# Optimization experiments

Hardware: AMD Instinct MI355X
Metric: run time of the kernel (lower is better)

Reference implementation:

```python
import jax, jax.numpy as jnp
import numpy as np

N_NODES = 50000
N_EDGES = 50000  # per-node attention scores are used as per-hyperedge weights => M == N
IN_CH = 128
OUT_CH = 128
NNZ = 800000


def setup_inputs() -> dict:
    key = jax.random.key(0)
    k = jax.random.split(key, 7)
    x = jax.random.normal(k[0], (N_NODES, IN_CH), dtype=jnp.float32)
    node_idx = jax.random.randint(k[1], (NNZ,), 0, N_NODES)
    edge_idx = jax.random.randint(k[2], (NNZ,), 0, N_EDGES)
    hyperedge_index = jnp.stack([node_idx, edge_idx]).astype(jnp.int64)
    s_in = 1.0 / np.sqrt(IN_CH)
    attn_w = jax.random.uniform(k[3], (1, IN_CH), minval=-s_in, maxval=s_in, dtype=jnp.float32)
    attn_b = jax.random.uniform(k[4], (1,), minval=-s_in, maxval=s_in, dtype=jnp.float32)
    lin_w = jax.random.uniform(k[5], (OUT_CH, IN_CH), minval=-s_in, maxval=s_in, dtype=jnp.float32)
    bias = jax.random.uniform(k[6], (OUT_CH,), minval=-s_in, maxval=s_in, dtype=jnp.float32)
    return {"x": x, "hyperedge_index": hyperedge_index,
            "attn_w": attn_w, "attn_b": attn_b, "lin_w": lin_w, "bias": bias}


def reference(x, hyperedge_index, attn_w, attn_b, lin_w, bias):
    # x: [N, C_in]; hyperedge_index: [2, nnz] (row 0: node ids, row 1: hyperedge ids)
    node_idx = hyperedge_index[0]
    edge_idx = hyperedge_index[1]
    N = x.shape[0]
    M = N_EDGES

    # edge_weight = sigmoid(attn(x)) -> used as hyperedge_weight (per-edge, M == N)
    w = jax.nn.sigmoid(x @ attn_w.T + attn_b)[:, 0]            # [M]

    xl = x @ lin_w.T                                           # [N, C_out]

    # D_v = sum of incident hyperedge weights per node; D^{-1} with inf -> 0
    D = jax.ops.segment_sum(w[edge_idx], node_idx, num_segments=N)
    Dinv = jnp.where(D > 0, 1.0 / D, 0.0)                      # [N]

    # B_e = hyperedge degree; B^{-1} with inf -> 0
    ones = jnp.ones(edge_idx.shape, dtype=x.dtype)
    Bdeg = jax.ops.segment_sum(ones, edge_idx, num_segments=M)
    Binv = jnp.where(Bdeg > 0, 1.0 / Bdeg, 0.0)                # [M]

    # node -> hyperedge: message = B_e^{-1} * x_j, aggregated at edge e
    msg = Binv[edge_idx][:, None] * xl[node_idx]               # [nnz, C_out]
    e_feat = jax.ops.segment_sum(msg, edge_idx, num_segments=M)

    # hyperedge -> node: message = D_v^{-1} * e_feat, aggregated at node v
    out = jax.ops.segment_sum(e_feat[edge_idx], node_idx, num_segments=N)
    out = Dinv[:, None] * out

    return out + bias
```

## Files before the change

### kernel.cpp

```cpp
#include <hip/hip_runtime.h>
#include <math.h>

#define CH 128
#define CAP 64
#define RSB 9
#define RS  (1 << RSB)
#define CAPB 10240
#define PB 2048
#define SUB 8
#define IDS 64

typedef __attribute__((ext_vector_type(8))) short bf16x8;
typedef __attribute__((ext_vector_type(4))) float f32x4;

__device__ __forceinline__ unsigned short f2bf(float f) {
    union { float f; unsigned u; } v; v.f = f;
    unsigned r = v.u + 0x7FFF + ((v.u >> 16) & 1);
    return (unsigned short)(r >> 16);
}
__device__ __forceinline__ float bflo(unsigned u) {
    union { unsigned u; float f; } v; v.u = u << 16; return v.f;
}
__device__ __forceinline__ float bfhi(unsigned u) {
    union { unsigned u; float f; } v; v.u = u & 0xFFFF0000u; return v.f;
}
__device__ __forceinline__ unsigned pack2bf(float a, float b) {
    return (unsigned)f2bf(a) | ((unsigned)f2bf(b) << 16);
}

__global__ __launch_bounds__(256) void fused_main(const float* __restrict__ x,
                                                  const float* __restrict__ attn_w,
                                                  const float* __restrict__ attn_b,
                                                  const float* __restrict__ lw,
                                                  unsigned short* __restrict__ xl,
                                                  float* __restrict__ w,
                                                  int nStrips,
                                                  const int* __restrict__ nidx,
                                                  const int* __restrict__ eidx,
                                                  int* __restrict__ binCnt,
                                                  unsigned int* __restrict__ binData,
                                                  int nnz, int nbd, int SB) {
    __shared__ unsigned short wl[128 * 136];
    __shared__ float awl[128];
    if ((int)blockIdx.x < SB) {
        int* hist = (int*)wl;
        int* base = ((int*)wl) + 256;
        int nbt = 2 * nbd;
        for (int i = threadIdx.x; i < nbt; i += 256) hist[i] = 0;
        __syncthreads();
        int k0 = blockIdx.x * PB + threadIdx.x;
        int vv[8], ee[8], sE[8], sN[8];
#pragma unroll
        for (int u = 0; u < 8; ++u) {
            int k = k0 + u * 256;
            if (k < nnz) {
                int v = nidx[k], e = eidx[k];
                vv[u] = v; ee[u] = e;
                sE[u] = atomicAdd(&hist[e >> RSB], 1);
                sN[u] = atomicAdd(&hist[nbd + (v >> RSB)], 1);
            } else vv[u] = -1;
        }
        __syncthreads();
        for (int i = threadIdx.x; i < nbt; i += 256)
            if (hist[i]) base[i] = atomicAdd(&binCnt[i], hist[i]);
        __syncthreads();
#pragma unroll
        for (int u = 0; u < 8; ++u) {
            if (vv[u] < 0) continue;
            int bE = ee[u] >> RSB;
            int bN = nbd + (vv[u] >> RSB);
            int iE = min(base[bE] + sE[u], CAPB - 1);
            int iN = min(base[bN] + sN[u], CAPB - 1);
            binData[(size_t)bE * CAPB + iE] = ((unsigned)ee[u] << 16) | (unsigned)vv[u];
            binData[(size_t)bN * CAPB + iN] = ((unsigned)vv[u] << 16) | (unsigned)ee[u];
        }
        return;
    }
    int tid = threadIdx.x;
    for (int i = tid; i < 2048; i += 256) {
        float4 vlo = ((const float4*)lw)[2 * i];
        float4 vhi = ((const float4*)lw)[2 * i + 1];
        int4 dst;
        dst.x = (int)pack2bf(vlo.x, vlo.y);
        dst.y = (int)pack2bf(vlo.z, vlo.w);
        dst.z = (int)pack2bf(vhi.x, vhi.y);
        dst.w = (int)pack2bf(vhi.z, vhi.w);
        *(int4*)(wl + (i >> 4) * 136 + (i & 15) * 8) = dst;
    }
    if (tid < 128) awl[tid] = attn_w[tid];
    float ab = attn_b[0];
    __syncthreads();
    int gb = blockIdx.x - SB;
    int wid = (gb << 2) | (tid >> 6);
    int lane = tid & 63;
    int m = lane & 15, quad = lane >> 4;
    int nWaves = ((int)gridDim.x - SB) << 2;
    for (int s = wid; s < nStrips; s += nWaves) {
        int r0 = s << 4;
        const float* xr = x + (size_t)(r0 + m) * CH + quad * 8;
        float att = 0.f;
        bf16x8 a0, a1, a2, a3;
#define LOAD_FRAG(AFRAG, F)                                                   \
        {                                                                     \
            float4 lo = *(const float4*)(xr + (F) * 32);                      \
            float4 hi = *(const float4*)(xr + (F) * 32 + 4);                  \
            const float* ap = &awl[(F) * 32 + quad * 8];                      \
            att += lo.x * ap[0] + lo.y * ap[1] + lo.z * ap[2] + lo.w * ap[3]  \
                 + hi.x * ap[4] + hi.y * ap[5] + hi.z * ap[6] + hi.w * ap[7]; \
            union { int4 i; bf16x8 v; } pk;                                   \
            pk.i.x = (int)pack2bf(lo.x, lo.y);                                \
            pk.i.y = (int)pack2bf(lo.z, lo.w);                                \
            pk.i.z = (int)pack2bf(hi.x, hi.y);                                \
            pk.i.w = (int)pack2bf(hi.z, hi.w);                                \
            AFRAG = pk.v;                                                     \
        }
        LOAD_FRAG(a0, 0)
        LOAD_FRAG(a1, 1)
        LOAD_FRAG(a2, 2)
        LOAD_FRAG(a3, 3)
#undef LOAD_FRAG
        att += __shfl_xor(att, 16, 64);
        att += __shfl_xor(att, 32, 64);
        if (quad == 0) w[r0 + m] = 1.0f / (1.0f + expf(-(att + ab)));
        unsigned short* orow = xl + (size_t)(r0 + quad * 4) * CH + m;
#pragma unroll
        for (int c0 = 0; c0 < 128; c0 += 16) {
            const unsigned short* wr = wl + (c0 + m) * 136 + quad * 8;
            f32x4 acc = {0.f, 0.f, 0.f, 0.f};
            acc = __builtin_amdgcn_mfma_f32_16x16x32_bf16(a0, *(const bf16x8*)(wr), acc, 0, 0, 0);
            acc = __builtin_amdgcn_mfma_f32_16x16x32_bf16(a1, *(const bf16x8*)(wr + 32), acc, 0, 0, 0);
            acc = __builtin_amdgcn_mfma_f32_16x16x32_bf16(a2, *(const bf16x8*)(wr + 64), acc, 0, 0, 0);
            acc = __builtin_amdgcn_mfma_f32_16x16x32_bf16(a3, *(const bf16x8*)(wr + 96), acc, 0, 0, 0);
            orow[c0]            = f2bf(acc[0]);
            orow[c0 + CH]       = f2bf(acc[1]);
            orow[c0 + 2 * CH]   = f2bf(acc[2]);
            orow[c0 + 3 * CH]   = f2bf(acc[3]);
        }
    }
}

__global__ __launch_bounds__(512) void edge_agg(const int* __restrict__ binCnt,
                                                const unsigned int* __restrict__ binData,
                                                const unsigned short* __restrict__ xl,
                                                unsigned short* __restrict__ ef, int M) {
    __shared__ unsigned short bucket[IDS * CAP];
    __shared__ int cl[IDS];
    int cb = blockIdx.x >> 3;
    int sr = blockIdx.x & (SUB - 1);
    int idBase = (cb << RSB) + (sr << 6);
    for (int i = threadIdx.x; i < IDS; i += 512) cl[i] = 0;
    __syncthreads();
    int n = min(binCnt[cb], CAPB);
    const unsigned int* src = binData + (size_t)cb * CAPB;
    for (int i = threadIdx.x; i < n; i += 512) {
        unsigned int entry = src[i];
        int lid = (int)(entry >> 16) - idBase;
        if ((unsigned)lid < IDS) {
            int r = atomicAdd(&cl[lid], 1);
            bucket[(lid << 6) + min(r, CAP - 1)] = (unsigned short)(entry & 0xFFFFu);
        }
    }
    __syncthreads();
    int wid = threadIdx.x >> 6, lane = threadIdx.x & 63;
    for (int li = wid; li < IDS; li += 8) {
        int gid = idBase + li;
        if (gid >= M) break;
        int deg = cl[li];
        int dl = min(deg, CAP);
        const unsigned short* col = bucket + (li << 6);
        float2 a0 = {0.f, 0.f}, a1 = {0.f, 0.f}, a2 = {0.f, 0.f}, a3 = {0.f, 0.f};
        int j = 0;
        for (; j + 3 < dl; j += 4) {
            int v0 = col[j], v1 = col[j + 1], v2 = col[j + 2], v3 = col[j + 3];
            unsigned u0 = *(const unsigned*)(xl + (size_t)v0 * CH + 2 * lane);
            unsigned u1 = *(const unsigned*)(xl + (size_t)v1 * CH + 2 * lane);
            unsigned u2 = *(const unsigned*)(xl + (size_t)v2 * CH + 2 * lane);
            unsigned u3 = *(const unsigned*)(xl + (size_t)v3 * CH + 2 * lane);
            a0.x += bflo(u0); a0.y += bfhi(u0);
            a1.x += bflo(u1); a1.y += bfhi(u1);
            a2.x += bflo(u2); a2.y += bfhi(u2);
            a3.x += bflo(u3); a3.y += bfhi(u3);
        }
        for (; j < dl; ++j) {
            unsigned u0 = *(const unsigned*)(xl + (size_t)col[j] * CH + 2 * lane);
            a0.x += bflo(u0); a0.y += bfhi(u0);
        }
        a0.x += a1.x + a2.x + a3.x;
        a0.y += a1.y + a2.y + a3.y;
        float binv = deg > 0 ? 1.0f / (float)deg : 0.0f;
        *(unsigned*)(ef + (size_t)gid * CH + 2 * lane) = pack2bf(a0.x * binv, a0.y * binv);
    }
}

__global__ __launch_bounds__(512) void node_agg(const int* __restrict__ binCnt,
                                                const unsigned int* __restrict__ binData,
                                                const unsigned short* __restrict__ ef,
                                                const float* __restrict__ w,
                                                const float* __restrict__ bias,
                                                float* __restrict__ out, int N) {
    __shared__ unsigned short bucket[IDS * CAP];
    __shared__ int cl[IDS];
    int cb = blockIdx.x >> 3;
    int sr = blockIdx.x & (SUB - 1);
    int idBase = (cb << RSB) + (sr << 6);
    for (int i = threadIdx.x; i < IDS; i += 512) cl[i] = 0;
    __syncthreads();
    int n = min(binCnt[cb], CAPB);
    const unsigned int* src = binData + (size_t)cb * CAPB;
    for (int i = threadIdx.x; i < n; i += 512) {
        unsigned int entry = src[i];
        int lid = (int)(entry >> 16) - idBase;
        if ((unsigned)lid < IDS) {
            int r = atomicAdd(&cl[lid], 1);
            bucket[(lid << 6) + min(r, CAP - 1)] = (unsigned short)(entry & 0xFFFFu);
        }
    }
    __syncthreads();
    int wid = threadIdx.x >> 6, lane = threadIdx.x & 63;
    for (int li = wid; li < IDS; li += 8) {
        int gid = idBase + li;
        if (gid >= N) break;
        int deg = cl[li];
        int dl = min(deg, CAP);
        const unsigned short* col = bucket + (li << 6);
        float2 a0 = {0.f, 0.f}, a1 = {0.f, 0.f}, a2 = {0.f, 0.f}, a3 = {0.f, 0.f};
        float ds = 0.f;
        int j = 0;
        for (; j + 3 < dl; j += 4) {
            int e0 = col[j], e1 = col[j + 1], e2 = col[j + 2], e3 = col[j + 3];
            unsigned u0 = *(const unsigned*)(ef + (size_t)e0 * CH + 2 * lane);
            unsigned u1 = *(const unsigned*)(ef + (size_t)e1 * CH + 2 * lane);
            unsigned u2 = *(const unsigned*)(ef + (size_t)e2 * CH + 2 * lane);
            unsigned u3 = *(const unsigned*)(ef + (size_t)e3 * CH + 2 * lane);
            ds += w[e0] + w[e1] + w[e2] + w[e3];
            a0.x += bflo(u0); a0.y += bfhi(u0);
            a1.x += bflo(u1); a1.y += bfhi(u1);
            a2.x += bflo(u2); a2.y += bfhi(u2);
            a3.x += bflo(u3); a3.y += bfhi(u3);
        }
        for (; j < dl; ++j) {
            int e0 = col[j];
            unsigned u0 = *(const unsigned*)(ef + (size_t)e0 * CH + 2 * lane);
            ds += w[e0];
            a0.x += bflo(u0); a0.y += bfhi(u0);
        }
        a0.x += a1.x + a2.x + a3.x;
        a0.y += a1.y + a2.y + a3.y;
        float dinv = ds > 0.f ? 1.0f / ds : 0.0f;
        float2 bi = *(const float2*)(bias + 2 * lane);
        float2 o = {a0.x * dinv + bi.x, a0.y * dinv + bi.y};
        *(float2*)(out + (size_t)gid * CH + 2 * lane) = o;
    }
}

extern "C" void kernel_launch(void* const* d_in, const int* in_sizes, int n_in,
                              void* d_out, int out_size, void* d_ws, size_t ws_size,
                              hipStream_t stream) {
    const float* x      = (const float*)d_in[0];
    const int*   hei    = (const int*)d_in[1];
    const float* attn_w = (const float*)d_in[2];
    const float* attn_b = (const float*)d_in[3];
    const float* lin_w  = (const float*)d_in[4];
    const float* bias   = (const float*)d_in[5];
    float* out = (float*)d_out;

    const int N   = in_sizes[0] / CH;
    const int nnz = in_sizes[1] / 2;
    const int* nidx = hei;
    const int* eidx = hei + nnz;

    unsigned short* efbf = (unsigned short*)d_ws;
    float*          w    = (float*)(efbf + (size_t)N * CH);
    unsigned int*   binData = (unsigned int*)(w + N);
    int nbd = (N + RS - 1) >> RSB;
    int*            binCnt  = (int*)(binData + (size_t)2 * nbd * CAPB);

    unsigned short* xlbf = (unsigned short*)out;

    hipMemsetAsync(binCnt, 0, (size_t)2 * nbd * sizeof(int), stream);

    int SB = (nnz + PB - 1) / PB;
    int nStrips = N / 16;
    int GB = (nStrips + 3) / 4;
    fused_main<<<SB + GB, 256, 0, stream>>>(x, attn_w, attn_b, lin_w, xlbf, w,
                                            nStrips, nidx, eidx, binCnt, binData,
                                            nnz, nbd, SB);

    edge_agg<<<nbd * SUB, 512, 0, stream>>>(binCnt, binData, xlbf, efbf, N);
    node_agg<<<nbd * SUB, 512, 0, stream>>>(binCnt + nbd,
                                            binData + (size_t)nbd * CAPB,
                                            efbf, w, bias, out, N);
}
```

Measured before the change: 180.3 us.

## Split wavefronts into half-waves gathering two rows each, double sub-bins per bin

Each wavefront now splits into two 32-lane halves that gather alternate neighbor rows with 8-byte loads, then combines them with a cross-half shuffle. The bin is split into 16 sub-ranges of 32 ids instead of 8 of 64, which doubles the block count, and the bin-scan loop reads entries as uint4. The goal is to raise memory-level parallelism and occupancy in the gather-bound aggregation kernels. In exchange, every block rescans the whole bin, so bin scanning is duplicated twice as often, and half the lanes sit idle during the final store.

```diff
diff --git a/kernel.cpp b/kernel.cpp
--- a/kernel.cpp
+++ b/kernel.cpp
@@ -7,8 +7,8 @@
 #define RS  (1 << RSB)
 #define CAPB 10240
 #define PB 2048
-#define SUB 8
-#define IDS 64
+#define SUB 16
+#define IDS 32
 
 typedef __attribute__((ext_vector_type(8))) short bf16x8;
 typedef __attribute__((ext_vector_type(4))) float f32x4;
@@ -139,117 +139,137 @@
     }
 }
 
-__global__ __launch_bounds__(512) void edge_agg(const int* __restrict__ binCnt,
-                                                const unsigned int* __restrict__ binData,
-                                                const unsigned short* __restrict__ xl,
-                                                unsigned short* __restrict__ ef, int M) {
+__global__ __launch_bounds__(512, 8) void edge_agg(const int* __restrict__ binCnt,
+                                                   const unsigned int* __restrict__ binData,
+                                                   const unsigned short* __restrict__ xl,
+                                                   unsigned short* __restrict__ ef, int M) {
     __shared__ unsigned short bucket[IDS * CAP];
     __shared__ int cl[IDS];
-    int cb = blockIdx.x >> 3;
+    int cb = blockIdx.x >> 4;
     int sr = blockIdx.x & (SUB - 1);
-    int idBase = (cb << RSB) + (sr << 6);
-    for (int i = threadIdx.x; i < IDS; i += 512) cl[i] = 0;
+    int idBase = (cb << RSB) + (sr << 5);
+    if (threadIdx.x < IDS) cl[threadIdx.x] = 0;
     __syncthreads();
     int n = min(binCnt[cb], CAPB);
     const unsigned int* src = binData + (size_t)cb * CAPB;
-    for (int i = threadIdx.x; i < n; i += 512) {
-        unsigned int entry = src[i];
-        int lid = (int)(entry >> 16) - idBase;
-        if ((unsigned)lid < IDS) {
-            int r = atomicAdd(&cl[lid], 1);
-            bucket[(lid << 6) + min(r, CAP - 1)] = (unsigned short)(entry & 0xFFFFu);
+    for (int i0 = (int)threadIdx.x << 2; i0 < n; i0 += 2048) {
+        if (i0 + 4 <= n) {
+            uint4 e4 = *(const uint4*)(src + i0);
+#define SCAN1(E) { int lid = (int)((E) >> 16) - idBase;                        \
+                   if ((unsigned)lid < IDS) {                                  \
+                       int r = atomicAdd(&cl[lid], 1);                         \
+                       bucket[(lid << 6) + min(r, CAP - 1)] =                  \
+                           (unsigned short)((E) & 0xFFFFu); } }
+            SCAN1(e4.x) SCAN1(e4.y) SCAN1(e4.z) SCAN1(e4.w)
+        } else {
+            for (int i = i0; i < n; ++i) { unsigned int e1 = src[i]; SCAN1(e1) }
         }
     }
     __syncthreads();
     int wid = threadIdx.x >> 6, lane = threadIdx.x & 63;
+    int half = lane >> 5, hl = lane & 31;
     for (int li = wid; li < IDS; li += 8) {
         int gid = idBase + li;
         if (gid >= M) break;
         int deg = cl[li];
         int dl = min(deg, CAP);
         const unsigned short* col = bucket + (li << 6);
-        float2 a0 = {0.f, 0.f}, a1 = {0.f, 0.f}, a2 = {0.f, 0.f}, a3 = {0.f, 0.f};
+        float4 acc = {0.f, 0.f, 0.f, 0.f};
+        int npair = dl >> 1;
         int j = 0;
-        for (; j + 3 < dl; j += 4) {
-            int v0 = col[j], v1 = col[j + 1], v2 = col[j + 2], v3 = col[j + 3];
-            unsigned u0 = *(const unsigned*)(xl + (size_t)v0 * CH + 2 * lane);
-            unsigned u1 = *(const unsigned*)(xl + (size_t)v1 * CH + 2 * lane);
-            unsigned u2 = *(const unsigned*)(xl + (size_t)v2 * CH + 2 * lane);
-            unsigned u3 = *(const unsigned*)(xl + (size_t)v3 * CH + 2 * lane);
-            a0.x += bflo(u0); a0.y += bfhi(u0);
-            a1.x += bflo(u1); a1.y += bfhi(u1);
-            a2.x += bflo(u2); a2.y += bfhi(u2);
-            a3.x += bflo(u3); a3.y += bfhi(u3);
-        }
-        for (; j < dl; ++j) {
-            unsigned u0 = *(const unsigned*)(xl + (size_t)col[j] * CH + 2 * lane);
-            a0.x += bflo(u0); a0.y += bfhi(u0);
-        }
-        a0.x += a1.x + a2.x + a3.x;
-        a0.y += a1.y + a2.y + a3.y;
-        float binv = deg > 0 ? 1.0f / (float)deg : 0.0f;
-        *(unsigned*)(ef + (size_t)gid * CH + 2 * lane) = pack2bf(a0.x * binv, a0.y * binv);
-    }
-}
-
-__global__ __launch_bounds__(512) void node_agg(const int* __restrict__ binCnt,
-                                                const unsigned int* __restrict__ binData,
-                                                const unsigned short* __restrict__ ef,
-                                                const float* __restrict__ w,
-                                                const float* __restrict__ bias,
-                                                float* __restrict__ out, int N) {
+#define ROW(MID) { uint2 u = *(const uint2*)(xl + (size_t)(MID) * CH + 4 * hl); \
+                   acc.x += bflo(u.x); acc.y += bfhi(u.x);                      \
+                   acc.z += bflo(u.y); acc.w += bfhi(u.y); }
+        for (; j + 4 <= npair; j += 4) {
+            int m0 = col[2 * j + half];
+            int m1 = col[2 * j + 2 + half];
+            int m2 = col[2 * j + 4 + half];
+            int m3 = col[2 * j + 6 + half];
+            ROW(m0) ROW(m1) ROW(m2) ROW(m3)
+        }
+        for (; j < npair; ++j) { int m0 = col[2 * j + half]; ROW(m0) }
+        if ((dl & 1) && half == 0) { int m0 = col[dl - 1]; ROW(m0) }
+#undef ROW
+        acc.x += __shfl_xor(acc.x, 32, 64);
+        acc.y += __shfl_xor(acc.y, 32, 64);
+        acc.z += __shfl_xor(acc.z, 32, 64);
+        acc.w += __shfl_xor(acc.w, 32, 64);
+        if (half == 0) {
+            float binv = deg > 0 ? 1.0f / (float)deg : 0.0f;
+            uint2 o;
+            o.x = pack2bf(acc.x * binv, acc.y * binv);
+            o.y = pack2bf(acc.z * binv, acc.w * binv);
+            *(uint2*)(ef + (size_t)gid * CH + 4 * hl) = o;
+        }
+    }
+}
+
+__global__ __launch_bounds__(512, 8) void node_agg(const int* __restrict__ binCnt,
+                                                   const unsigned int* __restrict__ binData,
+                                                   const unsigned short* __restrict__ ef,
+                                                   const float* __restrict__ w,
+                                                   const float* __restrict__ bias,
+                                                   float* __restrict__ out, int N) {
     __shared__ unsigned short bucket[IDS * CAP];
     __shared__ int cl[IDS];
-    int cb = blockIdx.x >> 3;
+    int cb = blockIdx.x >> 4;
     int sr = blockIdx.x & (SUB - 1);
-    int idBase = (cb << RSB) + (sr << 6);
-    for (int i = threadIdx.x; i < IDS; i += 512) cl[i] = 0;
+    int idBase = (cb << RSB) + (sr << 5);
+    if (threadIdx.x < IDS) cl[threadIdx.x] = 0;
     __syncthreads();
     int n = min(binCnt[cb], CAPB);
     const unsigned int* src = binData + (size_t)cb * CAPB;
-    for (int i = threadIdx.x; i < n; i += 512) {
-        unsigned int entry = src[i];
-        int lid = (int)(entry >> 16) - idBase;
-        if ((unsigned)lid < IDS) {
-            int r = atomicAdd(&cl[lid], 1);
-            bucket[(lid << 6) + min(r, CAP - 1)] = (unsigned short)(entry & 0xFFFFu);
-        }
-    }
+    for (int i0 = (int)threadIdx.x << 2; i0 < n; i0 += 2048) {
+        if (i0 + 4 <= n) {
+            uint4 e4 = *(const uint4*)(src + i0);
+            SCAN1(e4.x) SCAN1(e4.y) SCAN1(e4.z) SCAN1(e4.w)
+        } else {
+            for (int i = i0; i < n; ++i) { unsigned int e1 = src[i]; SCAN1(e1) }
+        }
+    }
+#undef SCAN1
     __syncthreads();
     int wid = threadIdx.x >> 6, lane = threadIdx.x & 63;
+    int half = lane >> 5, hl = lane & 31;
     for (int li = wid; li < IDS; li += 8) {
         int gid = idBase + li;
         if (gid >= N) break;
         int deg = cl[li];
         int dl = min(deg, CAP);
         const unsigned short* col = bucket + (li << 6);
-        float2 a0 = {0.f, 0.f}, a1 = {0.f, 0.f}, a2 = {0.f, 0.f}, a3 = {0.f, 0.f};
+        float4 acc = {0.f, 0.f, 0.f, 0.f};
         float ds = 0.f;
+        int npair = dl >> 1;
         int j = 0;
-        for (; j + 3 < dl; j += 4) {
-            int e0 = col[j], e1 = col[j + 1], e2 = col[j + 2], e3 = col[j + 3];
-            unsigned u0 = *(const unsigned*)(ef + (size_t)e0 * CH + 2 * lane);
-            unsigned u1 = *(const unsigned*)(ef + (size_t)e1 * CH + 2 * lane);
-            unsigned u2 = *(const unsigned*)(ef + (size_t)e2 * CH + 2 * lane);
-            unsigned u3 = *(const unsigned*)(ef + (size_t)e3 * CH + 2 * lane);
-            ds += w[e0] + w[e1] + w[e2] + w[e3];
-            a0.x += bflo(u0); a0.y += bfhi(u0);
-            a1.x += bflo(u1); a1.y += bfhi(u1);
-            a2.x += bflo(u2); a2.y += bfhi(u2);
-            a3.x += bflo(u3); a3.y += bfhi(u3);
-        }
-        for (; j < dl; ++j) {
-            int e0 = col[j];
-            unsigned u0 = *(const unsigned*)(ef + (size_t)e0 * CH + 2 * lane);
-            ds += w[e0];
-            a0.x += bflo(u0); a0.y += bfhi(u0);
-        }
-        a0.x += a1.x + a2.x + a3.x;
-        a0.y += a1.y + a2.y + a3.y;
-        float dinv = ds > 0.f ? 1.0f / ds : 0.0f;
-        float2 bi = *(const float2*)(bias + 2 * lane);
-        float2 o = {a0.x * dinv + bi.x, a0.y * dinv + bi.y};
-        *(float2*)(out + (size_t)gid * CH + 2 * lane) = o;
+#define ROW(MID) { uint2 u = *(const uint2*)(ef + (size_t)(MID) * CH + 4 * hl); \
+                   ds += w[MID];                                                \
+                   acc.x += bflo(u.x); acc.y += bfhi(u.x);                      \
+                   acc.z += bflo(u.y); acc.w += bfhi(u.y); }
+        for (; j + 4 <= npair; j += 4) {
+            int m0 = col[2 * j + half];
+            int m1 = col[2 * j + 2 + half];
+            int m2 = col[2 * j + 4 + half];
+            int m3 = col[2 * j + 6 + half];
+            ROW(m0) ROW(m1) ROW(m2) ROW(m3)
+        }
+        for (; j < npair; ++j) { int m0 = col[2 * j + half]; ROW(m0) }
+        if ((dl & 1) && half == 0) { int m0 = col[dl - 1]; ROW(m0) }
+#undef ROW
+        acc.x += __shfl_xor(acc.x, 32, 64);
+        acc.y += __shfl_xor(acc.y, 32, 64);
+        acc.z += __shfl_xor(acc.z, 32, 64);
+        acc.w += __shfl_xor(acc.w, 32, 64);
+        ds    += __shfl_xor(ds,    32, 64);
+        if (half == 0) {
+            float dinv = ds > 0.f ? 1.0f / ds : 0.0f;
+            float4 bi = *(const float4*)(bias + 4 * hl);
+            float4 o;
+            o.x = acc.x * dinv + bi.x;
+            o.y = acc.y * dinv + bi.y;
+            o.z = acc.z * dinv + bi.z;
+            o.w = acc.w * dinv + bi.w;
+            *(float4*)(out + (size_t)gid * CH + 4 * hl) = o;
+        }
     }
 }
 
```

Measured after the change: 176.1 us. -2.3%, faster.
